# Optimization experiments

Measured on AMD Instinct MI355X. Metric: run time of the kernel, lower is better.

Reference implementation:

```python
import jax, jax.numpy as jnp
import numpy as np

GAMMA = 2.0
EPS = 1e-06
LAMBDA_DISTANCE = 1.0
LAMBDA_NORMAL = 0.01
LAMBDA_LAPLACIAN = 0.1
CLS = 1


def vertex_normals(v, f, eps=EPS):
    # v: [N,3], f: [F,3] int. Scatter face normals to vertices, then normalize.
    fv = v[f]  # [F,3,3]
    fn = jnp.cross(fv[:, 1] - fv[:, 0], fv[:, 2] - fv[:, 0])  # [F,3]
    vn = jnp.zeros_like(v)
    vn = vn.at[f[:, 0]].add(fn).at[f[:, 1]].add(fn).at[f[:, 2]].add(fn)
    norm = jnp.maximum(jnp.linalg.norm(vn, axis=-1, keepdims=True), eps)
    return vn / norm


def squared_cdist(a, b):
    # [Na,3] x [Nb,3] -> squared euclidean distances [Na,Nb] (clamped >= 0)
    a2 = jnp.sum(a * a, axis=1)[:, None]
    b2 = jnp.sum(b * b, axis=1)[None, :]
    d2 = a2 + b2 - 2.0 * (a @ b.T)
    return jnp.maximum(d2, 0.0)


def sample_binary_targets(label, v, cls=CLS):
    # Nearest-neighbor grid_sample, align_corners=True, padding zeros.
    # grid = 2*v - 1 -> voxel index = round(v * (size-1)); v[:,0]->W, v[:,1]->H, v[:,2]->D.
    D, H, W = label.shape[2], label.shape[3], label.shape[4]
    ix = jnp.round(v[:, 0] * (W - 1)).astype(jnp.int32)
    iy = jnp.round(v[:, 1] * (H - 1)).astype(jnp.int32)
    iz = jnp.round(v[:, 2] * (D - 1)).astype(jnp.int32)
    inb = (ix >= 0) & (ix < W) & (iy >= 0) & (iy < H) & (iz >= 0) & (iz < D)
    ixc = jnp.clip(ix, 0, W - 1)
    iyc = jnp.clip(iy, 0, H - 1)
    izc = jnp.clip(iz, 0, D - 1)
    vals = (label[0, 0, izc, iyc, ixc] == cls).astype(jnp.float32)
    return jnp.where(inb, vals, 0.0)


def spatial_consistency_loss(rel_pos, targets, gamma=GAMMA, eps=EPS):
    p = jnp.clip(rel_pos, eps, 1.0 - eps)
    pos = targets > 0.5
    pc = jnp.sum(pos).astype(p.dtype)
    tot = jnp.asarray(p.shape[0], p.dtype)
    nc = tot - pc
    alpha = nc / (tot + eps)
    lpos = -alpha * jnp.power(1.0 - p, gamma) * jnp.log(p)
    lneg = -(1.0 - alpha) * jnp.power(p, gamma) * jnp.log(1.0 - p)
    return jnp.sum(jnp.where(pos, lpos, lneg)) / (tot + eps)


def laplacian_uniform(v, f):
    # Uniform mesh Laplacian smoothing: || mean(neighbors) - v ||, averaged.
    i = jnp.concatenate([f[:, 0], f[:, 1], f[:, 2], f[:, 1], f[:, 2], f[:, 0]])
    j = jnp.concatenate([f[:, 1], f[:, 2], f[:, 0], f[:, 0], f[:, 1], f[:, 2]])
    nsum = jnp.zeros_like(v).at[i].add(v[j])
    deg = jnp.zeros((v.shape[0],), v.dtype).at[i].add(1.0)
    lap = nsum / jnp.maximum(deg, 1.0)[:, None] - v
    return jnp.mean(jnp.linalg.norm(lap, axis=1))


def loss_forward(pred_vertices, relative_positions, gt_vertices, pred_faces, gt_faces, label):
    gt_v = jax.lax.stop_gradient(gt_vertices)  # gt comes from label volume; detached in original
    gt_normals = vertex_normals(gt_v, gt_faces)
    # spatial (focal-style) loss
    targets = sample_binary_targets(label, pred_vertices)
    spatial = spatial_consistency_loss(relative_positions, targets)
    # chamfer-style squared surface distance
    d2 = squared_cdist(pred_vertices, gt_v)  # [Np,Ng]
    distance = jnp.mean(jnp.min(d2, axis=1)) + jnp.mean(jnp.min(d2, axis=0))
    # normal consistency vs nearest gt vertex
    pred_normals = vertex_normals(pred_vertices, pred_faces)
    nearest = jnp.argmin(d2, axis=1)
    normal = jnp.mean((pred_normals - gt_normals[nearest]) ** 2)
    # uniform laplacian smoothing
    laplacian = laplacian_uniform(pred_vertices, pred_faces)
    total = spatial + LAMBDA_DISTANCE * distance + LAMBDA_NORMAL * normal + LAMBDA_LAPLACIAN * laplacian
    return total


def setup_inputs() -> dict:
    key = jax.random.key(0)
    k1, k2, k3, k4, k5, k6 = jax.random.split(key, 6)
    Np, Ng = 8192, 12000
    pred_vertices = jax.random.uniform(k1, (Np, 3), dtype=jnp.float32)
    relative_positions = jax.random.uniform(k2, (Np,), dtype=jnp.float32)
    gt_vertices = jax.random.uniform(k3, (Ng, 3), dtype=jnp.float32)
    pred_faces = jax.random.randint(k4, (2 * Np, 3), 0, Np, dtype=jnp.int32)
    gt_faces = jax.random.randint(k5, (2 * Ng, 3), 0, Ng, dtype=jnp.int32)
    label = jax.random.randint(k6, (1, 1, 96, 96, 96), 0, 2, dtype=jnp.int32)
    return {"pred_vertices": pred_vertices, "relative_positions": relative_positions,
            "gt_vertices": gt_vertices, "pred_faces": pred_faces,
            "gt_faces": gt_faces, "label": label}


def reference(pred_vertices, relative_positions, gt_vertices, pred_faces, gt_faces, label):
    return loss_forward(pred_vertices, relative_positions, gt_vertices, pred_faces, gt_faces, label)
```

## Files before the change

### kernel.cpp

```cpp
#include <hip/hip_runtime.h>
#include <math.h>

#define NP 8192
#define NG 12000
#define NFP 16384
#define NFG 24000
#define EPSF 1e-6f

static constexpr size_t OFF_ROWMIN = 0;
static constexpr size_t OFF_COLMIN = 65536;
static constexpr size_t OFF_GTN    = 113664;
static constexpr size_t OFF_PNN    = 257664;
static constexpr size_t OFF_NSUM   = 355968;
static constexpr size_t OFF_DEG    = 454272;
static constexpr size_t OFF_SCAL   = 487040;
#define N_ZERO 93352

__global__ __launch_bounds__(256) void init_kernel(unsigned long long* __restrict__ rowmin,
                                                   unsigned* __restrict__ colmin,
                                                   float* __restrict__ zero) {
    int i = blockIdx.x * 256 + threadIdx.x;
    if (i < NP) rowmin[i] = 0xFFFFFFFFFFFFFFFFULL;
    if (i < NG) colmin[i] = 0x7f800000u;
    if (i < N_ZERO) zero[i] = 0.0f;
}

__global__ __launch_bounds__(256) void faces_kernel(const float* __restrict__ pv,
                                                    const int* __restrict__ pf,
                                                    const float* __restrict__ gv,
                                                    const int* __restrict__ gf,
                                                    float* __restrict__ gtn,
                                                    float* __restrict__ pnn,
                                                    float* __restrict__ nsum,
                                                    float* __restrict__ deg) {
    int t = blockIdx.x * 256 + threadIdx.x;
    if (t < NFG) {
        int i0 = gf[3*t], i1 = gf[3*t+1], i2 = gf[3*t+2];
        float ax = gv[3*i0], ay = gv[3*i0+1], az = gv[3*i0+2];
        float bx = gv[3*i1], by = gv[3*i1+1], bz = gv[3*i1+2];
        float cx = gv[3*i2], cy = gv[3*i2+1], cz = gv[3*i2+2];
        float ux = bx-ax, uy = by-ay, uz = bz-az;
        float wx = cx-ax, wy = cy-ay, wz = cz-az;
        float nx = uy*wz - uz*wy, ny = uz*wx - ux*wz, nz = ux*wy - uy*wx;
        atomicAdd(&gtn[3*i0+0], nx); atomicAdd(&gtn[3*i0+1], ny); atomicAdd(&gtn[3*i0+2], nz);
        atomicAdd(&gtn[3*i1+0], nx); atomicAdd(&gtn[3*i1+1], ny); atomicAdd(&gtn[3*i1+2], nz);
        atomicAdd(&gtn[3*i2+0], nx); atomicAdd(&gtn[3*i2+1], ny); atomicAdd(&gtn[3*i2+2], nz);
    } else if (t < NFG + NFP) {
        int u = t - NFG;
        int i0 = pf[3*u], i1 = pf[3*u+1], i2 = pf[3*u+2];
        float ax = pv[3*i0], ay = pv[3*i0+1], az = pv[3*i0+2];
        float bx = pv[3*i1], by = pv[3*i1+1], bz = pv[3*i1+2];
        float cx = pv[3*i2], cy = pv[3*i2+1], cz = pv[3*i2+2];
        float ux = bx-ax, uy = by-ay, uz = bz-az;
        float wx = cx-ax, wy = cy-ay, wz = cz-az;
        float nx = uy*wz - uz*wy, ny = uz*wx - ux*wz, nz = ux*wy - uy*wx;
        atomicAdd(&pnn[3*i0+0], nx); atomicAdd(&pnn[3*i0+1], ny); atomicAdd(&pnn[3*i0+2], nz);
        atomicAdd(&pnn[3*i1+0], nx); atomicAdd(&pnn[3*i1+1], ny); atomicAdd(&pnn[3*i1+2], nz);
        atomicAdd(&pnn[3*i2+0], nx); atomicAdd(&pnn[3*i2+1], ny); atomicAdd(&pnn[3*i2+2], nz);
        atomicAdd(&nsum[3*i0+0], bx+cx); atomicAdd(&nsum[3*i0+1], by+cy); atomicAdd(&nsum[3*i0+2], bz+cz);
        atomicAdd(&nsum[3*i1+0], cx+ax); atomicAdd(&nsum[3*i1+1], cy+ay); atomicAdd(&nsum[3*i1+2], cz+az);
        atomicAdd(&nsum[3*i2+0], ax+bx); atomicAdd(&nsum[3*i2+1], ay+by); atomicAdd(&nsum[3*i2+2], az+bz);
        atomicAdd(&deg[i0], 2.0f); atomicAdd(&deg[i1], 2.0f); atomicAdd(&deg[i2], 2.0f);
    }
}

#define ROW_GROUPS 8
#define ROW_CHUNKS 64
#define ROW_CH 188
#define ROW_BLOCKS (ROW_GROUPS*ROW_CHUNKS)
#define COL_GROUPS 12
#define COL_CHUNKS 43
#define COL_CH 192
#define COL_BLOCKS (COL_GROUPS*COL_CHUNKS)

__global__ __launch_bounds__(256) void cdist_kernel(const float* __restrict__ pred,
                                                    const float* __restrict__ gt,
                                                    unsigned long long* __restrict__ rowmin,
                                                    unsigned* __restrict__ colmin) {
    __shared__ float4 s[COL_CH];
    int b = blockIdx.x;
    if (b < ROW_BLOCKS) {
        int group = b >> 6;
        int chunk = b & 63;
        int gbase = chunk * ROW_CH;
        for (int j = threadIdx.x; j < ROW_CH; j += 256) {
            int gj = gbase + j;
            if (gj < NG) {
                float x = gt[3*gj], y = gt[3*gj+1], z = gt[3*gj+2];
                s[j] = make_float4(x, y, z, fmaf(x,x, fmaf(y,y, z*z)));
            } else {
                s[j] = make_float4(0.f, 0.f, 0.f, 3.0e38f);
            }
        }
        __syncthreads();
        int pv0 = group * 1024 + threadIdx.x;
        float cx[4], cy[4], cz[4], a2[4], best[4];
        int bi[4];
        #pragma unroll
        for (int k = 0; k < 4; ++k) {
            int pv = pv0 + 256*k;
            float x = pred[3*pv], y = pred[3*pv+1], z = pred[3*pv+2];
            a2[k] = fmaf(x,x, fmaf(y,y, z*z));
            cx[k] = -2.0f*x; cy[k] = -2.0f*y; cz[k] = -2.0f*z;
            best[k] = 3.0e38f; bi[k] = 0;
        }
        #pragma unroll 4
        for (int j = 0; j < ROW_CH; ++j) {
            float4 q = s[j];
            #pragma unroll
            for (int k = 0; k < 4; ++k) {
                float t = fmaf(cx[k], q.x, fmaf(cy[k], q.y, fmaf(cz[k], q.z, q.w)));
                if (t < best[k]) { best[k] = t; bi[k] = gbase + j; }
            }
        }
        #pragma unroll
        for (int k = 0; k < 4; ++k) {
            float d2 = fmaxf(a2[k] + best[k], 0.0f);
            unsigned long long key =
                ((unsigned long long)__float_as_uint(d2) << 32) | (unsigned)bi[k];
            atomicMin(&rowmin[pv0 + 256*k], key);
        }
    } else {
        int bb = b - ROW_BLOCKS;
        int group = bb / COL_CHUNKS;
        int chunk = bb % COL_CHUNKS;
        int pbase = chunk * COL_CH;
        for (int j = threadIdx.x; j < COL_CH; j += 256) {
            int pj = pbase + j;
            if (pj < NP) {
                float x = pred[3*pj], y = pred[3*pj+1], z = pred[3*pj+2];
                s[j] = make_float4(x, y, z, fmaf(x,x, fmaf(y,y, z*z)));
            } else {
                s[j] = make_float4(0.f, 0.f, 0.f, 3.0e38f);
            }
        }
        __syncthreads();
        int gv0 = group * 1024 + threadIdx.x;
        float cx[4], cy[4], cz[4], a2[4], best[4];
        #pragma unroll
        for (int k = 0; k < 4; ++k) {
            int gv = gv0 + 256*k;
            float x = 0.f, y = 0.f, z = 0.f;
            if (gv < NG) { x = gt[3*gv]; y = gt[3*gv+1]; z = gt[3*gv+2]; }
            a2[k] = fmaf(x,x, fmaf(y,y, z*z));
            cx[k] = -2.0f*x; cy[k] = -2.0f*y; cz[k] = -2.0f*z;
            best[k] = 3.0e38f;
        }
        #pragma unroll 4
        for (int j = 0; j < COL_CH; ++j) {
            float4 q = s[j];
            #pragma unroll
            for (int k = 0; k < 4; ++k) {
                float t = fmaf(cx[k], q.x, fmaf(cy[k], q.y, fmaf(cz[k], q.z, q.w)));
                best[k] = fminf(best[k], t);
            }
        }
        #pragma unroll
        for (int k = 0; k < 4; ++k) {
            int gv = gv0 + 256*k;
            if (gv < NG) {
                float d2 = fmaxf(a2[k] + best[k], 0.0f);
                atomicMin(&colmin[gv], __float_as_uint(d2));
            }
        }
    }
}

__device__ __forceinline__ float wave_sum(float x) {
    #pragma unroll
    for (int o = 32; o > 0; o >>= 1) x += __shfl_down(x, o, 64);
    return x;
}

#define FIN_PRED_BLOCKS 32
#define FIN_COL_BLOCKS 47
__global__ __launch_bounds__(256) void finalize_kernel(const float* __restrict__ pred,
                                                       const float* __restrict__ relpos,
                                                       const int* __restrict__ label,
                                                       const unsigned long long* __restrict__ rowmin,
                                                       const unsigned* __restrict__ colmin,
                                                       const float* __restrict__ pnn,
                                                       const float* __restrict__ gtn,
                                                       const float* __restrict__ nsum,
                                                       const float* __restrict__ deg,
                                                       float* __restrict__ scal) {
    if (blockIdx.x < FIN_PRED_BLOCKS) {
        int v = blockIdx.x * 256 + threadIdx.x;
        unsigned long long key = rowmin[v];
        float dmin = __uint_as_float((unsigned)(key >> 32));
        int nearest = (int)(unsigned)(key & 0xffffffffu);
        float px = pred[3*v], py = pred[3*v+1], pz = pred[3*v+2];

        float ax = pnn[3*v], ay = pnn[3*v+1], az = pnn[3*v+2];
        float an = fmaxf(sqrtf(ax*ax + ay*ay + az*az), EPSF);
        float gx = gtn[3*nearest], gy = gtn[3*nearest+1], gz = gtn[3*nearest+2];
        float gn = fmaxf(sqrtf(gx*gx + gy*gy + gz*gz), EPSF);
        float nx = ax/an - gx/gn, ny = ay/an - gy/gn, nz = az/an - gz/gn;
        float sse = nx*nx + ny*ny + nz*nz;

        float d = fmaxf(deg[v], 1.0f);
        float lx = nsum[3*v]/d - px, ly = nsum[3*v+1]/d - py, lz = nsum[3*v+2]/d - pz;
        float lapn = sqrtf(lx*lx + ly*ly + lz*lz);

        int ix = (int)rintf(px * 95.0f), iy = (int)rintf(py * 95.0f), iz = (int)rintf(pz * 95.0f);
        bool inb = (ix >= 0) & (ix < 96) & (iy >= 0) & (iy < 96) & (iz >= 0) & (iz < 96);
        int ixc = min(max(ix, 0), 95), iyc = min(max(iy, 0), 95), izc = min(max(iz, 0), 95);
        bool pos = inb && (label[(izc*96 + iyc)*96 + ixc] == 1);

        float p = fminf(fmaxf(relpos[v], EPSF), 1.0f - EPSF);
        float om = 1.0f - p;
        float pcnt = 0.0f, sx = 0.0f, sy = 0.0f;
        if (pos) { pcnt = 1.0f; sx = om*om*logf(p); }
        else     { sy = p*p*logf(om); }

        float r0 = wave_sum(dmin);
        float r1 = wave_sum(sse);
        float r2 = wave_sum(lapn);
        float r3 = wave_sum(pcnt);
        float r4 = wave_sum(sx);
        float r5 = wave_sum(sy);
        if ((threadIdx.x & 63) == 0) {
            atomicAdd(&scal[0], r0);
            atomicAdd(&scal[5], r1);
            atomicAdd(&scal[6], r2);
            atomicAdd(&scal[2], r3);
            atomicAdd(&scal[3], r4);
            atomicAdd(&scal[4], r5);
        }
    } else {
        int gv = (blockIdx.x - FIN_PRED_BLOCKS) * 256 + threadIdx.x;
        float val = (gv < NG) ? __uint_as_float(colmin[gv]) : 0.0f;
        float r = wave_sum(val);
        if ((threadIdx.x & 63) == 0) atomicAdd(&scal[1], r);
    }
}

__global__ void combine_kernel(const float* __restrict__ scal, float* __restrict__ out) {
    float sum_row = scal[0], sum_col = scal[1];
    float pc = scal[2], SX = scal[3], SY = scal[4];
    float sse = scal[5], lap = scal[6];
    float tot = (float)NP;
    float alpha = (tot - pc) / (tot + EPSF);
    float spatial = (-alpha * SX - (1.0f - alpha) * SY) / (tot + EPSF);
    float distance = sum_row / (float)NP + sum_col / (float)NG;
    float normal = sse / (float)(NP * 3);
    float lapm = lap / (float)NP;
    out[0] = spatial + 1.0f * distance + 0.01f * normal + 0.1f * lapm;
}

extern "C" void kernel_launch(void* const* d_in, const int* in_sizes, int n_in,
                              void* d_out, int out_size, void* d_ws, size_t ws_size,
                              hipStream_t stream) {
    const float* pred   = (const float*)d_in[0];
    const float* relpos = (const float*)d_in[1];
    const float* gt     = (const float*)d_in[2];
    const int*   pfaces = (const int*)d_in[3];
    const int*   gfaces = (const int*)d_in[4];
    const int*   label  = (const int*)d_in[5];
    float* out = (float*)d_out;

    char* ws = (char*)d_ws;
    unsigned long long* rowmin = (unsigned long long*)(ws + OFF_ROWMIN);
    unsigned*           colmin = (unsigned*)(ws + OFF_COLMIN);
    float*              gtn    = (float*)(ws + OFF_GTN);
    float*              pnn    = (float*)(ws + OFF_PNN);
    float*              nsum   = (float*)(ws + OFF_NSUM);
    float*              deg    = (float*)(ws + OFF_DEG);
    float*              scal   = (float*)(ws + OFF_SCAL);

    hipLaunchKernelGGL(init_kernel, dim3((N_ZERO + 255) / 256), dim3(256), 0, stream,
                       rowmin, colmin, gtn);
    hipLaunchKernelGGL(faces_kernel, dim3((NFG + NFP + 255) / 256), dim3(256), 0, stream,
                       pred, pfaces, gt, gfaces, gtn, pnn, nsum, deg);
    hipLaunchKernelGGL(cdist_kernel, dim3(ROW_BLOCKS + COL_BLOCKS), dim3(256), 0, stream,
                       pred, gt, rowmin, colmin);
    hipLaunchKernelGGL(finalize_kernel, dim3(FIN_PRED_BLOCKS + FIN_COL_BLOCKS), dim3(256), 0, stream,
                       pred, relpos, label, rowmin, colmin, pnn, gtn, nsum, deg, scal);
    hipLaunchKernelGGL(combine_kernel, dim3(1), dim3(1), 0, stream, scal, out);
}
```

Baseline: 132.8 us.

## Fuse face-normal scatter into cdist kernel and combine into finalize via ticket

```diff
diff --git a/kernel.cpp b/kernel.cpp
--- a/kernel.cpp
+++ b/kernel.cpp
@@ -25,45 +25,6 @@
     if (i < N_ZERO) zero[i] = 0.0f;
 }
 
-__global__ __launch_bounds__(256) void faces_kernel(const float* __restrict__ pv,
-                                                    const int* __restrict__ pf,
-                                                    const float* __restrict__ gv,
-                                                    const int* __restrict__ gf,
-                                                    float* __restrict__ gtn,
-                                                    float* __restrict__ pnn,
-                                                    float* __restrict__ nsum,
-                                                    float* __restrict__ deg) {
-    int t = blockIdx.x * 256 + threadIdx.x;
-    if (t < NFG) {
-        int i0 = gf[3*t], i1 = gf[3*t+1], i2 = gf[3*t+2];
-        float ax = gv[3*i0], ay = gv[3*i0+1], az = gv[3*i0+2];
-        float bx = gv[3*i1], by = gv[3*i1+1], bz = gv[3*i1+2];
-        float cx = gv[3*i2], cy = gv[3*i2+1], cz = gv[3*i2+2];
-        float ux = bx-ax, uy = by-ay, uz = bz-az;
-        float wx = cx-ax, wy = cy-ay, wz = cz-az;
-        float nx = uy*wz - uz*wy, ny = uz*wx - ux*wz, nz = ux*wy - uy*wx;
-        atomicAdd(&gtn[3*i0+0], nx); atomicAdd(&gtn[3*i0+1], ny); atomicAdd(&gtn[3*i0+2], nz);
-        atomicAdd(&gtn[3*i1+0], nx); atomicAdd(&gtn[3*i1+1], ny); atomicAdd(&gtn[3*i1+2], nz);
-        atomicAdd(&gtn[3*i2+0], nx); atomicAdd(&gtn[3*i2+1], ny); atomicAdd(&gtn[3*i2+2], nz);
-    } else if (t < NFG + NFP) {
-        int u = t - NFG;
-        int i0 = pf[3*u], i1 = pf[3*u+1], i2 = pf[3*u+2];
-        float ax = pv[3*i0], ay = pv[3*i0+1], az = pv[3*i0+2];
-        float bx = pv[3*i1], by = pv[3*i1+1], bz = pv[3*i1+2];
-        float cx = pv[3*i2], cy = pv[3*i2+1], cz = pv[3*i2+2];
-        float ux = bx-ax, uy = by-ay, uz = bz-az;
-        float wx = cx-ax, wy = cy-ay, wz = cz-az;
-        float nx = uy*wz - uz*wy, ny = uz*wx - ux*wz, nz = ux*wy - uy*wx;
-        atomicAdd(&pnn[3*i0+0], nx); atomicAdd(&pnn[3*i0+1], ny); atomicAdd(&pnn[3*i0+2], nz);
-        atomicAdd(&pnn[3*i1+0], nx); atomicAdd(&pnn[3*i1+1], ny); atomicAdd(&pnn[3*i1+2], nz);
-        atomicAdd(&pnn[3*i2+0], nx); atomicAdd(&pnn[3*i2+1], ny); atomicAdd(&pnn[3*i2+2], nz);
-        atomicAdd(&nsum[3*i0+0], bx+cx); atomicAdd(&nsum[3*i0+1], by+cy); atomicAdd(&nsum[3*i0+2], bz+cz);
-        atomicAdd(&nsum[3*i1+0], cx+ax); atomicAdd(&nsum[3*i1+1], cy+ay); atomicAdd(&nsum[3*i1+2], cz+az);
-        atomicAdd(&nsum[3*i2+0], ax+bx); atomicAdd(&nsum[3*i2+1], ay+by); atomicAdd(&nsum[3*i2+2], az+bz);
-        atomicAdd(&deg[i0], 2.0f); atomicAdd(&deg[i1], 2.0f); atomicAdd(&deg[i2], 2.0f);
-    }
-}
-
 #define ROW_GROUPS 8
 #define ROW_CHUNKS 64
 #define ROW_CH 188
@@ -72,11 +33,19 @@
 #define COL_CHUNKS 43
 #define COL_CH 192
 #define COL_BLOCKS (COL_GROUPS*COL_CHUNKS)
-
-__global__ __launch_bounds__(256) void cdist_kernel(const float* __restrict__ pred,
-                                                    const float* __restrict__ gt,
-                                                    unsigned long long* __restrict__ rowmin,
-                                                    unsigned* __restrict__ colmin) {
+#define CD_BLOCKS (ROW_BLOCKS + COL_BLOCKS)
+#define FACE_BLOCKS ((NFG + NFP + 255) / 256)
+
+__global__ __launch_bounds__(256) void mega_kernel(const float* __restrict__ pred,
+                                                   const int* __restrict__ pf,
+                                                   const float* __restrict__ gt,
+                                                   const int* __restrict__ gf,
+                                                   unsigned long long* __restrict__ rowmin,
+                                                   unsigned* __restrict__ colmin,
+                                                   float* __restrict__ gtn,
+                                                   float* __restrict__ pnn,
+                                                   float* __restrict__ nsum,
+                                                   float* __restrict__ deg) {
     __shared__ float4 s[COL_CH];
     int b = blockIdx.x;
     if (b < ROW_BLOCKS) {
@@ -120,7 +89,7 @@
                 ((unsigned long long)__float_as_uint(d2) << 32) | (unsigned)bi[k];
             atomicMin(&rowmin[pv0 + 256*k], key);
         }
-    } else {
+    } else if (b < CD_BLOCKS) {
         int bb = b - ROW_BLOCKS;
         int group = bb / COL_CHUNKS;
         int chunk = bb % COL_CHUNKS;
@@ -163,6 +132,36 @@
                 atomicMin(&colmin[gv], __float_as_uint(d2));
             }
         }
+    } else {
+        int t = (b - CD_BLOCKS) * 256 + threadIdx.x;
+        if (t < NFG) {
+            int i0 = gf[3*t], i1 = gf[3*t+1], i2 = gf[3*t+2];
+            float ax = gt[3*i0], ay = gt[3*i0+1], az = gt[3*i0+2];
+            float bx = gt[3*i1], by = gt[3*i1+1], bz = gt[3*i1+2];
+            float cx = gt[3*i2], cy = gt[3*i2+1], cz = gt[3*i2+2];
+            float ux = bx-ax, uy = by-ay, uz = bz-az;
+            float wx = cx-ax, wy = cy-ay, wz = cz-az;
+            float nx = uy*wz - uz*wy, ny = uz*wx - ux*wz, nz = ux*wy - uy*wx;
+            atomicAdd(&gtn[3*i0+0], nx); atomicAdd(&gtn[3*i0+1], ny); atomicAdd(&gtn[3*i0+2], nz);
+            atomicAdd(&gtn[3*i1+0], nx); atomicAdd(&gtn[3*i1+1], ny); atomicAdd(&gtn[3*i1+2], nz);
+            atomicAdd(&gtn[3*i2+0], nx); atomicAdd(&gtn[3*i2+1], ny); atomicAdd(&gtn[3*i2+2], nz);
+        } else if (t < NFG + NFP) {
+            int u = t - NFG;
+            int i0 = pf[3*u], i1 = pf[3*u+1], i2 = pf[3*u+2];
+            float ax = pred[3*i0], ay = pred[3*i0+1], az = pred[3*i0+2];
+            float bx = pred[3*i1], by = pred[3*i1+1], bz = pred[3*i1+2];
+            float cx = pred[3*i2], cy = pred[3*i2+1], cz = pred[3*i2+2];
+            float ux = bx-ax, uy = by-ay, uz = bz-az;
+            float wx = cx-ax, wy = cy-ay, wz = cz-az;
+            float nx = uy*wz - uz*wy, ny = uz*wx - ux*wz, nz = ux*wy - uy*wx;
+            atomicAdd(&pnn[3*i0+0], nx); atomicAdd(&pnn[3*i0+1], ny); atomicAdd(&pnn[3*i0+2], nz);
+            atomicAdd(&pnn[3*i1+0], nx); atomicAdd(&pnn[3*i1+1], ny); atomicAdd(&pnn[3*i1+2], nz);
+            atomicAdd(&pnn[3*i2+0], nx); atomicAdd(&pnn[3*i2+1], ny); atomicAdd(&pnn[3*i2+2], nz);
+            atomicAdd(&nsum[3*i0+0], bx+cx); atomicAdd(&nsum[3*i0+1], by+cy); atomicAdd(&nsum[3*i0+2], bz+cz);
+            atomicAdd(&nsum[3*i1+0], cx+ax); atomicAdd(&nsum[3*i1+1], cy+ay); atomicAdd(&nsum[3*i1+2], cz+az);
+            atomicAdd(&nsum[3*i2+0], ax+bx); atomicAdd(&nsum[3*i2+1], ay+by); atomicAdd(&nsum[3*i2+2], az+bz);
+            atomicAdd(&deg[i0], 2.0f); atomicAdd(&deg[i1], 2.0f); atomicAdd(&deg[i2], 2.0f);
+        }
     }
 }
 
@@ -174,6 +173,7 @@
 
 #define FIN_PRED_BLOCKS 32
 #define FIN_COL_BLOCKS 47
+#define FIN_TOTAL (FIN_PRED_BLOCKS + FIN_COL_BLOCKS)
 __global__ __launch_bounds__(256) void finalize_kernel(const float* __restrict__ pred,
                                                        const float* __restrict__ relpos,
                                                        const int* __restrict__ label,
@@ -183,7 +183,9 @@
                                                        const float* __restrict__ gtn,
                                                        const float* __restrict__ nsum,
                                                        const float* __restrict__ deg,
-                                                       float* __restrict__ scal) {
+                                                       float* __restrict__ scal,
+                                                       unsigned* __restrict__ ticket,
+                                                       float* __restrict__ out) {
     if (blockIdx.x < FIN_PRED_BLOCKS) {
         int v = blockIdx.x * 256 + threadIdx.x;
         unsigned long long key = rowmin[v];
@@ -233,19 +235,30 @@
         float r = wave_sum(val);
         if ((threadIdx.x & 63) == 0) atomicAdd(&scal[1], r);
     }
-}
-
-__global__ void combine_kernel(const float* __restrict__ scal, float* __restrict__ out) {
-    float sum_row = scal[0], sum_col = scal[1];
-    float pc = scal[2], SX = scal[3], SY = scal[4];
-    float sse = scal[5], lap = scal[6];
-    float tot = (float)NP;
-    float alpha = (tot - pc) / (tot + EPSF);
-    float spatial = (-alpha * SX - (1.0f - alpha) * SY) / (tot + EPSF);
-    float distance = sum_row / (float)NP + sum_col / (float)NG;
-    float normal = sse / (float)(NP * 3);
-    float lapm = lap / (float)NP;
-    out[0] = spatial + 1.0f * distance + 0.01f * normal + 0.1f * lapm;
+
+    __threadfence();
+    __shared__ int is_last;
+    if (threadIdx.x == 0) {
+        unsigned t = atomicAdd(ticket, 1u);
+        is_last = (t == FIN_TOTAL - 1) ? 1 : 0;
+    }
+    __syncthreads();
+    if (is_last && threadIdx.x == 0) {
+        float sum_row = atomicAdd(&scal[0], 0.0f);
+        float sum_col = atomicAdd(&scal[1], 0.0f);
+        float pc      = atomicAdd(&scal[2], 0.0f);
+        float SX      = atomicAdd(&scal[3], 0.0f);
+        float SY      = atomicAdd(&scal[4], 0.0f);
+        float sse     = atomicAdd(&scal[5], 0.0f);
+        float lap     = atomicAdd(&scal[6], 0.0f);
+        float tot = (float)NP;
+        float alpha = (tot - pc) / (tot + EPSF);
+        float spatial = (-alpha * SX - (1.0f - alpha) * SY) / (tot + EPSF);
+        float distance = sum_row / (float)NP + sum_col / (float)NG;
+        float normal = sse / (float)(NP * 3);
+        float lapm = lap / (float)NP;
+        out[0] = spatial + 1.0f * distance + 0.01f * normal + 0.1f * lapm;
+    }
 }
 
 extern "C" void kernel_launch(void* const* d_in, const int* in_sizes, int n_in,
@@ -267,14 +280,13 @@
     float*              nsum   = (float*)(ws + OFF_NSUM);
     float*              deg    = (float*)(ws + OFF_DEG);
     float*              scal   = (float*)(ws + OFF_SCAL);
+    unsigned*           ticket = (unsigned*)(ws + OFF_SCAL + 7*sizeof(float));
 
     hipLaunchKernelGGL(init_kernel, dim3((N_ZERO + 255) / 256), dim3(256), 0, stream,
                        rowmin, colmin, gtn);
-    hipLaunchKernelGGL(faces_kernel, dim3((NFG + NFP + 255) / 256), dim3(256), 0, stream,
-                       pred, pfaces, gt, gfaces, gtn, pnn, nsum, deg);
-    hipLaunchKernelGGL(cdist_kernel, dim3(ROW_BLOCKS + COL_BLOCKS), dim3(256), 0, stream,
-                       pred, gt, rowmin, colmin);
-    hipLaunchKernelGGL(finalize_kernel, dim3(FIN_PRED_BLOCKS + FIN_COL_BLOCKS), dim3(256), 0, stream,
-                       pred, relpos, label, rowmin, colmin, pnn, gtn, nsum, deg, scal);
-    hipLaunchKernelGGL(combine_kernel, dim3(1), dim3(1), 0, stream, scal, out);
-}
+    hipLaunchKernelGGL(mega_kernel, dim3(CD_BLOCKS + FACE_BLOCKS), dim3(256), 0, stream,
+                       pred, pfaces, gt, gfaces, rowmin, colmin, gtn, pnn, nsum, deg);
+    hipLaunchKernelGGL(finalize_kernel, dim3(FIN_TOTAL), dim3(256), 0, stream,
+                       pred, relpos, label, rowmin, colmin, pnn, gtn, nsum, deg,
+                       scal, ticket, out);
+}
```

Result: faster. 120.2 us (-9.5%).
